# Performance work log

Hardware: AMD Instinct MI355X
Metric: run time of the kernel (lower is better)

The kernel has to match this reference:

```python
import jax, jax.numpy as jnp
import numpy as np

DIM = 1024
NUM_HEADS = 16
HEAD_DIM = DIM // NUM_HEADS


def setup_inputs() -> dict:
    key = jax.random.key(0)
    k1, k2, k3, k4, k5 = jax.random.split(key, 5)
    s = 0.02
    return {
        "x": jax.random.normal(k1, (2, 2048, DIM), dtype=jnp.float32),
        "Wq": jax.random.normal(k2, (DIM, DIM), dtype=jnp.float32) * s,
        "Wk": jax.random.normal(k3, (DIM, DIM), dtype=jnp.float32) * s,
        "Wv": jax.random.normal(k4, (DIM, DIM), dtype=jnp.float32) * s,
        "Wo": jax.random.normal(k5, (DIM, DIM), dtype=jnp.float32) * s,
    }


def rotate_half(x):
    x1, x2 = x[..., : x.shape[-1] // 2], x[..., x.shape[-1] // 2 :]
    return jnp.concatenate([-x2, x1], axis=-1)


def rope_cos_sin(seq_len, head_dim, dtype):
    inv_freq = 1.0 / (10000.0 ** (jnp.arange(0, head_dim, 2, dtype=jnp.float32) / head_dim))
    t = jnp.arange(seq_len, dtype=jnp.float32)
    freqs = jnp.einsum("i,j->ij", t, inv_freq)  # [S, head_dim/2]
    emb = jnp.concatenate([freqs, freqs], axis=-1)  # [S, head_dim]
    return jnp.cos(emb).astype(dtype), jnp.sin(emb).astype(dtype)


def reference(x, Wq, Wk, Wv, Wo):
    B, S, D = x.shape
    H, Hd = NUM_HEADS, HEAD_DIM
    scale = Hd ** -0.5

    def proj(W):
        # nn.Linear: x @ W.T; reshape to [B, H, S, Hd]
        return (x @ W.T).reshape(B, S, H, Hd).transpose(0, 2, 1, 3)

    q, k, v = proj(Wq), proj(Wk), proj(Wv)
    cos, sin = rope_cos_sin(S, Hd, x.dtype)  # [S, Hd], broadcast over B,H
    q = q * cos + rotate_half(q) * sin
    k = k * cos + rotate_half(k) * sin

    attn = jnp.einsum("bhqd,bhkd->bhqk", q, k) * scale  # [B,H,S,S]
    causal = jnp.triu(jnp.ones((S, S), dtype=bool), k=1)
    attn = jnp.where(causal, -jnp.inf, attn)
    attn = jax.nn.softmax(attn, axis=-1)
    out = jnp.einsum("bhqk,bhkd->bhqd", attn, v)
    out = out.transpose(0, 2, 1, 3).reshape(B, S, D)
    return out @ Wo.T
```

## Files before the change

kernel.cpp:

```cpp
#include <hip/hip_runtime.h>

#define DIM 1024
#define NHEADS 16
#define HD 64
#define SEQ 2048
#define BATCH 2
#define MROWS (BATCH*SEQ)
#define QKVLD 3072

typedef _Float16 h16;
typedef __attribute__((ext_vector_type(2))) _Float16 h16x2;
typedef __attribute__((ext_vector_type(2))) __fp16 fp16x2;
typedef __attribute__((ext_vector_type(4))) _Float16 h16x4;
typedef __attribute__((ext_vector_type(8))) _Float16 h16x8;
typedef __attribute__((ext_vector_type(4))) float f32x4;
typedef __attribute__((ext_vector_type(16))) float f32x16;

union U2 { fp16x2 g; h16x2 h; unsigned u; };

#define CBAR() do { asm volatile("" ::: "memory"); __builtin_amdgcn_s_barrier(); \
                    asm volatile("" ::: "memory"); } while (0)

__global__ __launch_bounds__(256) void prep_k(
    const float* __restrict__ x,  const float* __restrict__ wq,
    const float* __restrict__ wk, const float* __restrict__ wv,
    const float* __restrict__ wo,
    h16* __restrict__ xh, h16* __restrict__ wqkvh, h16* __restrict__ woh,
    float2* __restrict__ rope)
{
    const int NX = MROWS * DIM / 4;
    const int NW = DIM * DIM / 4;
    int gid = blockIdx.x * 256 + threadIdx.x;
    if (gid < NX) {
        float4 v = *reinterpret_cast<const float4*>(x + (size_t)gid * 4);
        h16x4 o; o.x=(h16)v.x; o.y=(h16)v.y; o.z=(h16)v.z; o.w=(h16)v.w;
        *reinterpret_cast<h16x4*>(xh + (size_t)gid * 4) = o;
    } else if (gid < NX + 3 * NW) {
        int j = gid - NX;
        int w = j >> 18, e = j & (NW - 1);
        const float* s = (w == 0) ? wq : (w == 1) ? wk : wv;
        float4 v = *reinterpret_cast<const float4*>(s + (size_t)e * 4);
        h16x4 o; o.x=(h16)v.x; o.y=(h16)v.y; o.z=(h16)v.z; o.w=(h16)v.w;
        *reinterpret_cast<h16x4*>(wqkvh + (size_t)w * DIM * DIM + (size_t)e * 4) = o;
    } else if (gid < NX + 4 * NW) {
        int e = gid - NX - 3 * NW;
        float4 v = *reinterpret_cast<const float4*>(wo + (size_t)e * 4);
        h16x4 o; o.x=(h16)v.x; o.y=(h16)v.y; o.z=(h16)v.z; o.w=(h16)v.w;
        *reinterpret_cast<h16x4*>(woh + (size_t)e * 4) = o;
    } else {
        int t = gid - NX - 4 * NW;
        int s = t >> 5, j = t & 31;
        float inv = powf(10000.0f, -(float)j / 32.0f);
        float ang = (float)s * inv;
        rope[t] = make_float2(cosf(ang), sinf(ang));
    }
}

__global__ __launch_bounds__(512, 2) void gemm256_qkv(
    const h16* __restrict__ A, const h16* __restrict__ Bw,
    h16* __restrict__ C, const float2* __restrict__ rope)
{
    __shared__ h16 As[2][256][64];
    __shared__ h16 Bs[2][256][64];
    const int tid = threadIdx.x, wave = tid >> 6, lane = tid & 63;
    const int lr = lane & 15, lg = lane >> 4;
    const int wm = wave >> 2, wn = wave & 3;
    const int ntn = QKVLD >> 8;
    const int bm = blockIdx.x / ntn, bn = blockIdx.x % ntn;
    const int m0 = bm << 8, n0 = bn << 8;

    const int srl = lane >> 3;
    const int sgc = ((lane & 7) ^ srl) << 3;

#define STAGE_HALF(buf, k0_, h_) do {                                               \
    _Pragma("unroll")                                                               \
    for (int j_ = 0; j_ < 2; ++j_) {                                                \
        int rl_ = ((h_) & 1) * 128 + (j_ * 8 + wave) * 8;                           \
        if ((h_) < 2) {                                                             \
            const h16* g_ = A + (size_t)(m0 + rl_ + srl) * DIM + (k0_) + sgc;       \
            __builtin_amdgcn_global_load_lds(                                       \
                (const __attribute__((address_space(1))) void*)g_,                  \
                (__attribute__((address_space(3))) void*)(&As[buf][rl_][0]), 16, 0, 0); \
        } else {                                                                    \
            const h16* g_ = Bw + (size_t)(n0 + rl_ + srl) * DIM + (k0_) + sgc;      \
            __builtin_amdgcn_global_load_lds(                                       \
                (const __attribute__((address_space(1))) void*)g_,                  \
                (__attribute__((address_space(3))) void*)(&Bs[buf][rl_][0]), 16, 0, 0); \
        }                                                                           \
    }                                                                               \
} while (0)

    f32x4 acc[8][4];
#pragma unroll
    for (int i = 0; i < 8; ++i)
#pragma unroll
        for (int j = 0; j < 4; ++j) acc[i][j] = (f32x4){0.f, 0.f, 0.f, 0.f};

    const int NT = DIM >> 6;
#pragma unroll
    for (int h = 0; h < 4; ++h) STAGE_HALF(0, 0, h);

    int cur = 0;
    for (int t = 0; t < NT; ++t) {
        const int k0n = (t + 1) << 6;
        const bool pf = (t + 1 < NT);
        h16x8 bfr[4][2];
#pragma unroll
        for (int p = 0; p < 4; ++p) {
            if (pf) STAGE_HALF(cur ^ 1, k0n, p);
            if (p == 0) {
                if (pf) asm volatile("s_waitcnt vmcnt(2)" ::: "memory");
                else    asm volatile("s_waitcnt vmcnt(0)" ::: "memory");
                CBAR();
            }
            h16x8 afr[2][2];
#pragma unroll
            for (int e = 0; e < 2; ++e)
#pragma unroll
                for (int ks = 0; ks < 2; ++ks) {
                    int r = wm * 128 + (2 * p + e) * 16 + lr;
                    int cpos = ((ks << 2) + lg) ^ (lr & 7);
                    afr[e][ks] = *(const h16x8*)&As[cur][r][cpos << 3];
                }
            if (p == 0) {
#pragma unroll
                for (int ni = 0; ni < 4; ++ni)
#pragma unroll
                    for (int ks = 0; ks < 2; ++ks) {
                        int r = wn * 64 + ni * 16 + lr;
                        int cpos = ((ks << 2) + lg) ^ (lr & 7);
                        bfr[ni][ks] = *(const h16x8*)&Bs[cur][r][cpos << 3];
                    }
            } else {
                CBAR();
            }
            __builtin_amdgcn_s_setprio(1);
#pragma unroll
            for (int e = 0; e < 2; ++e)
#pragma unroll
                for (int ni = 0; ni < 4; ++ni)
#pragma unroll
                    for (int ks = 0; ks < 2; ++ks)
                        acc[2 * p + e][ni] = __builtin_amdgcn_mfma_f32_16x16x32_f16(
                            afr[e][ks], bfr[ni][ks], acc[2 * p + e][ni], 0, 0, 0);
            __builtin_amdgcn_s_setprio(0);
            CBAR();
        }
        cur ^= 1;
    }
#undef STAGE_HALF

    const int region = n0 >> 10;
    if (region == 2) {
#pragma unroll
        for (int mi = 0; mi < 8; ++mi)
#pragma unroll
            for (int i = 0; i < 4; ++i) {
                int row = m0 + wm * 128 + mi * 16 + lg * 4 + i;
#pragma unroll
                for (int ni = 0; ni < 4; ++ni) {
                    int col = n0 + wn * 64 + ni * 16 + lr;
                    C[(size_t)row * QKVLD + col] = (h16)acc[mi][ni][i];
                }
            }
    } else {
#pragma unroll
        for (int mi = 0; mi < 8; ++mi)
#pragma unroll
            for (int i = 0; i < 4; ++i) {
                int row = m0 + wm * 128 + mi * 16 + lg * 4 + i;
                int s = row & (SEQ - 1);
#pragma unroll
                for (int ni = 0; ni < 4; ++ni) {
                    int col = n0 + wn * 64 + ni * 16 + lr;
                    int d = col & 63;
                    float2 cs = rope[(s << 5) + (d & 31)];
                    float v  = acc[mi][ni][i];
                    float vp = acc[mi][ni ^ 2][i];
                    float rh = (d < 32) ? -vp : vp;
                    C[(size_t)row * QKVLD + col] = (h16)(v * cs.x + rh * cs.y);
                }
            }
    }
}

__global__ __launch_bounds__(256) void gemm_out(
    const h16* __restrict__ A, const h16* __restrict__ Bw,
    float* __restrict__ C, int M, int N, int K)
{
    __shared__ h16 As[128][64];
    __shared__ h16 Bs[128][64];
    const int tid  = threadIdx.x;
    const int wave = tid >> 6, lane = tid & 63;
    const int lr = lane & 15, lg = lane >> 4;
    const int wm = wave >> 1, wn = wave & 1;
    const int ntn = N >> 7;
    const int bm = blockIdx.x / ntn, bn = blockIdx.x % ntn;
    const int m0 = bm << 7, n0 = bn << 7;

    f32x4 acc[4][4];
#pragma unroll
    for (int i = 0; i < 4; ++i)
#pragma unroll
        for (int j = 0; j < 4; ++j) acc[i][j] = (f32x4){0.f, 0.f, 0.f, 0.f};

    const int arow = lane >> 3;
    const int acol = (lane & 7) << 3;

    for (int k0 = 0; k0 < K; k0 += 64) {
#pragma unroll
        for (int q = 0; q < 4; ++q) {
            int ch = wave * 4 + q;
            const h16* ga = A + (size_t)(m0 + ch * 8 + arow) * K + k0 + acol;
            __builtin_amdgcn_global_load_lds(
                (const __attribute__((address_space(1))) void*)ga,
                (__attribute__((address_space(3))) void*)(&As[ch * 8][0]), 16, 0, 0);
            const h16* gb = Bw + (size_t)(n0 + ch * 8 + arow) * K + k0 + acol;
            __builtin_amdgcn_global_load_lds(
                (const __attribute__((address_space(1))) void*)gb,
                (__attribute__((address_space(3))) void*)(&Bs[ch * 8][0]), 16, 0, 0);
        }
        __syncthreads();
#pragma unroll
        for (int ks = 0; ks < 2; ++ks) {
            h16x8 af[4], bf[4];
#pragma unroll
            for (int mi = 0; mi < 4; ++mi)
                af[mi] = *(const h16x8*)&As[wm * 64 + mi * 16 + lr][ks * 32 + lg * 8];
#pragma unroll
            for (int ni = 0; ni < 4; ++ni)
                bf[ni] = *(const h16x8*)&Bs[wn * 64 + ni * 16 + lr][ks * 32 + lg * 8];
#pragma unroll
            for (int mi = 0; mi < 4; ++mi)
#pragma unroll
                for (int ni = 0; ni < 4; ++ni)
                    acc[mi][ni] = __builtin_amdgcn_mfma_f32_16x16x32_f16(
                        af[mi], bf[ni], acc[mi][ni], 0, 0, 0);
        }
        __syncthreads();
    }

#pragma unroll
    for (int mi = 0; mi < 4; ++mi)
#pragma unroll
        for (int i = 0; i < 4; ++i) {
            int row = m0 + wm * 64 + mi * 16 + lg * 4 + i;
#pragma unroll
            for (int ni = 0; ni < 4; ++ni) {
                int col = n0 + wn * 64 + ni * 16 + lr;
                C[(size_t)row * N + col] = acc[mi][ni][i];
            }
        }
}

__global__ __launch_bounds__(512) void attn_k(
    const h16* __restrict__ QKV, h16* __restrict__ O)
{
    __shared__ h16 Ks[2][64][64];
    __shared__ h16 Vt[2][64][72];

    const int bx = blockIdx.x, by = blockIdx.y;
    const int b = by >> 4, h = by & 15;
    const int tid = threadIdx.x, wave = tid >> 6, lane = tid & 63;
    const int lq = lane & 31, hi = lane >> 5;
    const int qlo = bx, qhi = 15 - bx;

    const h16* Qb = QKV + (size_t)b * SEQ * QKVLD + h * HD;
    const h16* Kb = Qb + DIM;
    const h16* Vb = Qb + 2 * DIM;

    const int qw0 = (wave < 4) ? (qlo * 128 + wave * 32)
                               : (qhi * 128 + (wave - 4) * 32);

    h16x8 qf[4];
    {
        const h16* qp = Qb + (size_t)(qw0 + lq) * QKVLD + 8 * hi;
        const h16 qs = (h16)(0.125f * 1.44269504f);
#pragma unroll
        for (int kb = 0; kb < 4; ++kb) {
            qf[kb] = *(const h16x8*)(qp + 16 * kb);
            qf[kb] *= qs;
        }
    }

    float l_run = 0.f;
    f32x16 accd[2];
#pragma unroll
    for (int i = 0; i < 16; ++i) { accd[0][i] = 0.f; accd[1][i] = 0.f; }

    const int kwave = wave - 4;
    const int kr = (tid & 255) >> 3, kc = tid & 7;
    h16x8 vv0, vv1;

#define STAGE_K(bufi, kv0_) do {                                                   \
    const h16* gk0_ = Kb + (size_t)((kv0_) + kr) * QKVLD + ((kc ^ (kr & 7)) << 3); \
    __builtin_amdgcn_global_load_lds(                                              \
        (const __attribute__((address_space(1))) void*)gk0_,                       \
        (__attribute__((address_space(3))) void*)(&Ks[bufi][kwave * 8][0]), 16, 0, 0); \
    const h16* gk1_ = Kb + (size_t)((kv0_) + 32 + kr) * QKVLD + ((kc ^ (kr & 7)) << 3); \
    __builtin_amdgcn_global_load_lds(                                              \
        (const __attribute__((address_space(1))) void*)gk1_,                       \
        (__attribute__((address_space(3))) void*)(&Ks[bufi][32 + kwave * 8][0]), 16, 0, 0); \
} while (0)

#define VLOAD(kv0_) do {                                                           \
    const h16* gv_ = Vb + (size_t)((kv0_) + lane) * QKVLD + 16 * wave;             \
    vv0 = *(const h16x8*)gv_; vv1 = *(const h16x8*)(gv_ + 8);                      \
} while (0)

#define VWRITE(bufi) do {                                                          \
    _Pragma("unroll")                                                              \
    for (int j_ = 0; j_ < 8; ++j_) {                                               \
        Vt[bufi][16 * wave + j_][lane] = vv0[j_];                                  \
        Vt[bufi][16 * wave + 8 + j_][lane] = vv1[j_];                              \
    }                                                                              \
} while (0)

    const int nkv = 2 * qhi + 2;
    if (wave >= 4) STAGE_K(0, 0);
    else { VLOAD(0); VWRITE(0); }
    __syncthreads();

    for (int t = 0; t < nkv; ++t) {
        const int cur = t & 1;
        const int kv0 = t << 6;
        const bool pf = (t + 1 < nkv);
        if (pf) {
            if (wave >= 4) STAGE_K(cur ^ 1, kv0 + 64);
            else VLOAD(kv0 + 64);
        }

        const bool act = (kv0 <= qw0 + 31);
        float p[32];
        if (act) {
            f32x16 s0, s1;
#pragma unroll
            for (int i = 0; i < 16; ++i) { s0[i] = 0.f; s1[i] = 0.f; }
            const int sk = lq & 7;
            __builtin_amdgcn_s_setprio(1);
#pragma unroll
            for (int kb = 0; kb < 4; ++kb) {
                const int ch = ((2 * kb + hi) ^ sk) << 3;
                h16x8 kf0 = *(const h16x8*)&Ks[cur][lq][ch];
                h16x8 kf1 = *(const h16x8*)&Ks[cur][32 + lq][ch];
                s0 = __builtin_amdgcn_mfma_f32_32x32x16_f16(kf0, qf[kb], s0, 0, 0, 0);
                s1 = __builtin_amdgcn_mfma_f32_32x32x16_f16(kf1, qf[kb], s1, 0, 0, 0);
            }
            __builtin_amdgcn_s_setprio(0);
            const bool full = (kv0 + 64 <= qw0);
            float ls = 0.f;
            if (full) {
#pragma unroll
                for (int r = 0; r < 16; ++r) {
                    p[r]      = exp2f(s0[r]);
                    p[16 + r] = exp2f(s1[r]);
                    ls += p[r] + p[16 + r];
                }
            } else {
                const int Lq = qw0 + lq - kv0;
#pragma unroll
                for (int r = 0; r < 16; ++r) {
                    const int kvl = (r & 3) + 8 * (r >> 2) + 4 * hi;
                    float e0 = exp2f(s0[r]);
                    float e1 = exp2f(s1[r]);
                    p[r]      = (kvl <= Lq)      ? e0 : 0.f;
                    p[16 + r] = (kvl + 32 <= Lq) ? e1 : 0.f;
                    ls += p[r] + p[16 + r];
                }
            }
            l_run += ls;
        }
        if (pf && wave < 4) VWRITE(cur ^ 1);
        if (act) {
            h16x8 pfrag[4];
#pragma unroll
            for (int kva = 0; kva < 2; ++kva) {
                const int o = 16 * kva;
                U2 x, y, z, w, x2, y2, z2, w2;
                x.g  = __builtin_amdgcn_cvt_pkrtz(p[o+0],  p[o+1]);
                y.g  = __builtin_amdgcn_cvt_pkrtz(p[o+2],  p[o+3]);
                z.g  = __builtin_amdgcn_cvt_pkrtz(p[o+4],  p[o+5]);
                w.g  = __builtin_amdgcn_cvt_pkrtz(p[o+6],  p[o+7]);
                x2.g = __builtin_amdgcn_cvt_pkrtz(p[o+8],  p[o+9]);
                y2.g = __builtin_amdgcn_cvt_pkrtz(p[o+10], p[o+11]);
                z2.g = __builtin_amdgcn_cvt_pkrtz(p[o+12], p[o+13]);
                w2.g = __builtin_amdgcn_cvt_pkrtz(p[o+14], p[o+15]);
                asm volatile("v_permlane32_swap_b32 %0, %1" : "+v"(x.u),  "+v"(z.u));
                asm volatile("v_permlane32_swap_b32 %0, %1" : "+v"(y.u),  "+v"(w.u));
                asm volatile("v_permlane32_swap_b32 %0, %1" : "+v"(x2.u), "+v"(z2.u));
                asm volatile("v_permlane32_swap_b32 %0, %1" : "+v"(y2.u), "+v"(w2.u));
                h16x8 f0, f1;
                f0[0]=x.h.x;  f0[1]=x.h.y;  f0[2]=y.h.x;  f0[3]=y.h.y;
                f0[4]=z.h.x;  f0[5]=z.h.y;  f0[6]=w.h.x;  f0[7]=w.h.y;
                f1[0]=x2.h.x; f1[1]=x2.h.y; f1[2]=y2.h.x; f1[3]=y2.h.y;
                f1[4]=z2.h.x; f1[5]=z2.h.y; f1[6]=w2.h.x; f1[7]=w2.h.y;
                pfrag[2*kva]   = f0;
                pfrag[2*kva+1] = f1;
            }
            __builtin_amdgcn_s_setprio(1);
#pragma unroll
            for (int da = 0; da < 2; ++da)
#pragma unroll
                for (int kvb = 0; kvb < 4; ++kvb) {
                    h16x8 vf = *(const h16x8*)&Vt[cur][32 * da + lq][16 * kvb + 8 * hi];
                    accd[da] = __builtin_amdgcn_mfma_f32_32x32x16_f16(vf, pfrag[kvb], accd[da], 0, 0, 0);
                }
            __builtin_amdgcn_s_setprio(0);
        }
        __syncthreads();
    }

    float lt = l_run + __shfl_xor(l_run, 32);
    float inv = 1.0f / lt;
    h16* Ob = O + (size_t)b * SEQ * DIM + h * HD + (size_t)(qw0 + lq) * DIM;
#pragma unroll
    for (int da = 0; da < 2; ++da)
#pragma unroll
        for (int r = 0; r < 16; r += 2) {
            int d = 32 * da + (r & 3) + 8 * (r >> 2) + 4 * hi;
            h16x2 ov;
            ov.x = (h16)(accd[da][r] * inv);
            ov.y = (h16)(accd[da][r + 1] * inv);
            *(h16x2*)(Ob + d) = ov;
        }
#undef STAGE_K
#undef VLOAD
#undef VWRITE
}

extern "C" void kernel_launch(void* const* d_in, const int* in_sizes, int n_in,
                              void* d_out, int out_size, void* d_ws, size_t ws_size,
                              hipStream_t stream)
{
    const float* x  = (const float*)d_in[0];
    const float* Wq = (const float*)d_in[1];
    const float* Wk = (const float*)d_in[2];
    const float* Wv = (const float*)d_in[3];
    const float* Wo = (const float*)d_in[4];

    char* ws = (char*)d_ws;
    h16* xh     = (h16*)(ws);
    h16* wqkvh  = (h16*)(ws + ((size_t)8  << 20));
    h16* woh    = (h16*)(ws + ((size_t)14 << 20));
    h16* QKVd   = (h16*)(ws + ((size_t)16 << 20));
    h16* Od     = (h16*)(ws + ((size_t)40 << 20));
    float2* rope = (float2*)(ws + ((size_t)48 << 20));

    const int NX = MROWS * DIM / 4, NW = DIM * DIM / 4;
    prep_k<<<(NX + 4 * NW + SEQ * 32) / 256, 256, 0, stream>>>(
        x, Wq, Wk, Wv, Wo, xh, wqkvh, woh, rope);

    gemm256_qkv<<<(MROWS / 256) * (QKVLD / 256), 512, 0, stream>>>(
        xh, wqkvh, QKVd, rope);

    attn_k<<<dim3(8, BATCH * NHEADS), 512, 0, stream>>>(QKVd, Od);

    gemm_out<<<(MROWS / 128) * (DIM / 128), 256, 0, stream>>>(
        Od, woh, (float*)d_out, MROWS, DIM, DIM);
}
```

Before: 142.0 us.

## Double-buffer output GEMM staging and swizzle block order in both GEMMs

The output-projection GEMM gets double-buffered LDS tiles: the next K-tile's global-to-LDS loads are issued before the current tile's MFMAs, so load latency overlaps compute and one barrier per iteration is dropped. Both the QKV and output GEMMs also remap blockIdx into grouped tiles, so neighbouring blocks share A and B panels and L2 reuse should improve. The cost is twice the LDS in gemm_out, which may reduce occupancy. The block mappings hard-code grid shapes (32x8 tiles for out, 16x12 for QKV).

Result: no change. 140.7 us (-1.0%).

```diff
diff --git a/kernel.cpp b/kernel.cpp
--- a/kernel.cpp
+++ b/kernel.cpp
@@ -65,8 +65,9 @@
     const int tid = threadIdx.x, wave = tid >> 6, lane = tid & 63;
     const int lr = lane & 15, lg = lane >> 4;
     const int wm = wave >> 2, wn = wave & 3;
-    const int ntn = QKVLD >> 8;
-    const int bm = blockIdx.x / ntn, bn = blockIdx.x % ntn;
+    const int xr = blockIdx.x & 7, jr = blockIdx.x >> 3;
+    const int bm = ((xr >> 1) << 2) + (jr & 3);
+    const int bn = (xr & 1) * 6 + (jr >> 2);
     const int m0 = bm << 8, n0 = bn << 8;
 
     const int srl = lane >> 3;
@@ -188,14 +189,15 @@
     const h16* __restrict__ A, const h16* __restrict__ Bw,
     float* __restrict__ C, int M, int N, int K)
 {
-    __shared__ h16 As[128][64];
-    __shared__ h16 Bs[128][64];
+    __shared__ h16 As[2][128][64];
+    __shared__ h16 Bs[2][128][64];
     const int tid  = threadIdx.x;
     const int wave = tid >> 6, lane = tid & 63;
     const int lr = lane & 15, lg = lane >> 4;
     const int wm = wave >> 1, wn = wave & 1;
-    const int ntn = N >> 7;
-    const int bm = blockIdx.x / ntn, bn = blockIdx.x % ntn;
+    const int xr = blockIdx.x & 7, jr = blockIdx.x >> 3;
+    const int bm = ((xr >> 1) << 3) + (jr & 7);
+    const int bn = ((xr & 1) << 2) + (jr >> 3);
     const int m0 = bm << 7, n0 = bn << 7;
 
     f32x4 acc[4][4];
@@ -207,29 +209,36 @@
     const int arow = lane >> 3;
     const int acol = (lane & 7) << 3;
 
-    for (int k0 = 0; k0 < K; k0 += 64) {
-#pragma unroll
-        for (int q = 0; q < 4; ++q) {
-            int ch = wave * 4 + q;
-            const h16* ga = A + (size_t)(m0 + ch * 8 + arow) * K + k0 + acol;
-            __builtin_amdgcn_global_load_lds(
-                (const __attribute__((address_space(1))) void*)ga,
-                (__attribute__((address_space(3))) void*)(&As[ch * 8][0]), 16, 0, 0);
-            const h16* gb = Bw + (size_t)(n0 + ch * 8 + arow) * K + k0 + acol;
-            __builtin_amdgcn_global_load_lds(
-                (const __attribute__((address_space(1))) void*)gb,
-                (__attribute__((address_space(3))) void*)(&Bs[ch * 8][0]), 16, 0, 0);
-        }
-        __syncthreads();
+#define GSTAGE(buf, k0_) do {                                                      \
+    _Pragma("unroll")                                                              \
+    for (int q_ = 0; q_ < 4; ++q_) {                                               \
+        int ch_ = wave * 4 + q_;                                                   \
+        const h16* ga_ = A + (size_t)(m0 + ch_ * 8 + arow) * K + (k0_) + acol;     \
+        __builtin_amdgcn_global_load_lds(                                          \
+            (const __attribute__((address_space(1))) void*)ga_,                    \
+            (__attribute__((address_space(3))) void*)(&As[buf][ch_ * 8][0]), 16, 0, 0); \
+        const h16* gb_ = Bw + (size_t)(n0 + ch_ * 8 + arow) * K + (k0_) + acol;    \
+        __builtin_amdgcn_global_load_lds(                                          \
+            (const __attribute__((address_space(1))) void*)gb_,                    \
+            (__attribute__((address_space(3))) void*)(&Bs[buf][ch_ * 8][0]), 16, 0, 0); \
+    }                                                                              \
+} while (0)
+
+    const int NT = K >> 6;
+    GSTAGE(0, 0);
+    __syncthreads();
+    int cur = 0;
+    for (int t = 0; t < NT; ++t) {
+        if (t + 1 < NT) GSTAGE(cur ^ 1, (t + 1) << 6);
 #pragma unroll
         for (int ks = 0; ks < 2; ++ks) {
             h16x8 af[4], bf[4];
 #pragma unroll
             for (int mi = 0; mi < 4; ++mi)
-                af[mi] = *(const h16x8*)&As[wm * 64 + mi * 16 + lr][ks * 32 + lg * 8];
+                af[mi] = *(const h16x8*)&As[cur][wm * 64 + mi * 16 + lr][ks * 32 + lg * 8];
 #pragma unroll
             for (int ni = 0; ni < 4; ++ni)
-                bf[ni] = *(const h16x8*)&Bs[wn * 64 + ni * 16 + lr][ks * 32 + lg * 8];
+                bf[ni] = *(const h16x8*)&Bs[cur][wn * 64 + ni * 16 + lr][ks * 32 + lg * 8];
 #pragma unroll
             for (int mi = 0; mi < 4; ++mi)
 #pragma unroll
@@ -238,7 +247,9 @@
                         af[mi], bf[ni], acc[mi][ni], 0, 0, 0);
         }
         __syncthreads();
-    }
+        cur ^= 1;
+    }
+#undef GSTAGE
 
 #pragma unroll
     for (int mi = 0; mi < 4; ++mi)
```
